# Kernel tuning notes

Measured on AMD Instinct MI355X. Metric: run time of the kernel, lower is better.

## Reference

```python
import jax, jax.numpy as jnp
import numpy as np

N_VIEWS = 3
N = 20000            # samples per omic view
NT = N_VIEWS * N     # homogeneous node count
E = 800000           # number of edges
R = 6                # num_relations
B = 4                # num_bases
H = 1                # heads
D = 128              # proj_dim == hidden_channels
IN_FEAT = 2000
NUM_LABELS = 5
NEG_SLOPE = 0.2      # PyG leaky_relu default slope


def setup_inputs() -> dict:
    key = jax.random.key(0)
    ks = jax.random.split(key, 16)
    inp = {}
    for i in range(N_VIEWS):
        inp[f"x{i}"] = jax.random.normal(ks[i], (N, IN_FEAT), jnp.float32)
        inp[f"w_proj{i}"] = jax.random.normal(ks[3 + i], (IN_FEAT, D), jnp.float32) / np.sqrt(IN_FEAT)
        inp[f"b_proj{i}"] = jnp.zeros((D,), jnp.float32)
    inp["edge_src"] = jax.random.randint(ks[6], (E,), 0, NT, jnp.int32)
    inp["edge_dst"] = jax.random.randint(ks[7], (E,), 0, NT, jnp.int32)
    inp["edge_type"] = jax.random.randint(ks[8], (E,), 0, R, jnp.int32)
    inp["basis"] = jax.random.normal(ks[9], (B, D, H * D), jnp.float32) / np.sqrt(D)
    inp["comp"] = jax.random.normal(ks[10], (R, B), jnp.float32) / np.sqrt(B)
    inp["att_q"] = jax.random.normal(ks[11], (H * D, H), jnp.float32) / np.sqrt(D)
    inp["att_k"] = jax.random.normal(ks[12], (H * D, H), jnp.float32) / np.sqrt(D)
    inp["conv_bias"] = jnp.zeros((H * D,), jnp.float32)
    inp["w_int"] = jax.random.normal(ks[13], (N_VIEWS * H * D, NUM_LABELS), jnp.float32) / np.sqrt(N_VIEWS * D)
    inp["b_int"] = jnp.zeros((NUM_LABELS,), jnp.float32)
    return inp


def rgat_conv(x, edge_src, edge_dst, edge_type, basis, comp, att_q, att_k, bias):
    """PyG RGATConv: basis-decomposed relational transform + additive
    across-relation self-attention (dim=1), sum aggregation, concat heads."""
    e = edge_src.shape[0]
    # relation weights from bases: [R, D, H*D]
    w = jnp.einsum('rb,bio->rio', comp, basis)
    # transform every node under every relation: [R, NT, H*D]
    xw = jnp.einsum('nd,rdo->rno', x, w)
    xi = xw[edge_type, edge_dst]   # [E, H*D] transformed target feats
    xj = xw[edge_type, edge_src]   # [E, H*D] transformed source feats
    q = xi @ att_q                 # [E, H]
    k = xj @ att_k                 # [E, H]
    alpha = jax.nn.leaky_relu(q + k, NEG_SLOPE)
    # softmax over incoming edges of each target node (across relations)
    amax = jax.lax.stop_gradient(jax.ops.segment_max(alpha, edge_dst, num_segments=NT))
    ealpha = jnp.exp(alpha - amax[edge_dst])
    denom = jax.ops.segment_sum(ealpha, edge_dst, num_segments=NT)
    alpha = ealpha / (denom[edge_dst] + 1e-16)
    msg = (xj.reshape(e, H, D) * alpha[:, :, None]).reshape(e, H * D)
    out = jax.ops.segment_sum(msg, edge_dst, num_segments=NT)  # [NT, H*D]
    return out + bias


def reference(x0, x1, x2, w_proj0, b_proj0, w_proj1, b_proj1, w_proj2, b_proj2,
              edge_src, edge_dst, edge_type, basis, comp, att_q, att_k,
              conv_bias, w_int, b_int):
    # per-omic projection + relu, then concat to homogeneous node matrix
    h = jnp.concatenate([
        jax.nn.relu(x0 @ w_proj0 + b_proj0),
        jax.nn.relu(x1 @ w_proj1 + b_proj1),
        jax.nn.relu(x2 @ w_proj2 + b_proj2),
    ], axis=0)                                        # [NT, D]
    h = jax.nn.relu(rgat_conv(h, edge_src, edge_dst, edge_type,
                              basis, comp, att_q, att_k, conv_bias))
    # node-type gather: nodes are ordered by type in the homogeneous graph
    views = h.reshape(N_VIEWS, N, H * D)              # [V, N, D]
    feat = jnp.transpose(views, (1, 0, 2)).reshape(N, N_VIEWS * H * D)
    # LinearIntegration: concat views -> linear to classes
    return feat @ w_int + b_int                        # [N, NUM_LABELS]
```

## Files before the change

### kernel.cpp

```cpp
#include <hip/hip_runtime.h>

#define NV 3
#define NN 20000
#define NTT 60000
#define NE 800000
#define NR 6
#define NB 4
#define DD 128
#define INF 2000
#define NL 5
#define LDT 40

typedef __attribute__((ext_vector_type(8))) short short8;
typedef __attribute__((ext_vector_type(4))) float f32x4;

__device__ __forceinline__ unsigned short f2bf(float f) {
    unsigned int u = __float_as_uint(f);
    u += 0x7FFFu + ((u >> 16) & 1u);
    return (unsigned short)(u >> 16);
}
__device__ __forceinline__ float bf2f(unsigned short h) {
    return __uint_as_float(((unsigned int)h) << 16);
}


__global__ void prep_wT(const float* __restrict__ w0, const float* __restrict__ w1,
                        const float* __restrict__ w2, unsigned short* __restrict__ wT) {
    int idx = blockIdx.x * 256 + threadIdx.x;
    if (idx >= NV * DD * INF) return;
    int v = idx / (DD * INF);
    int rem = idx - v * DD * INF;
    int n = rem / INF;
    int k = rem - n * INF;
    const float* w = (v == 0) ? w0 : ((v == 1) ? w1 : w2);
    wT[idx] = f2bf(w[(size_t)k * DD + n]);
}

__global__ void prep_wrel(const float* __restrict__ basis, const float* __restrict__ comp,
                          unsigned short* __restrict__ wTrel) {
    int idx = blockIdx.x * 256 + threadIdx.x;
    if (idx >= NR * DD * DD) return;
    int r = idx / (DD * DD);
    int rem = idx - r * DD * DD;
    int o = rem / DD;
    int d = rem - o * DD;
    float s = 0.f;
    #pragma unroll
    for (int b = 0; b < NB; b++) s += comp[r * NB + b] * basis[((size_t)b * DD + d) * DD + o];
    wTrel[idx] = f2bf(s);
}

__global__ void prep_qkvec(const float* __restrict__ basis, const float* __restrict__ comp,
                           const float* __restrict__ att_q, const float* __restrict__ att_k,
                           float* __restrict__ qvec, float* __restrict__ kvec) {
    int idx = blockIdx.x * 256 + threadIdx.x;
    if (idx >= 2 * NR * DD) return;
    int sel = idx / (NR * DD);
    int rem = idx - sel * (NR * DD);
    int r = rem / DD;
    int d = rem - r * DD;
    const float* att = sel ? att_k : att_q;
    float s = 0.f;
    #pragma unroll
    for (int b = 0; b < NB; b++) {
        float cb = comp[r * NB + b];
        float t = 0.f;
        for (int o = 0; o < DD; o++) t += basis[((size_t)b * DD + d) * DD + o] * att[o];
        s += cb * t;
    }
    (sel ? kvec : qvec)[r * DD + d] = s;
}

__global__ void zero2(int* __restrict__ a, int* __restrict__ b) {
    int i = blockIdx.x * 256 + threadIdx.x;
    if (i < NTT) { a[i] = 0; b[i] = 0; }
}

__global__ __launch_bounds__(256) void proj_gemm(
    const float* __restrict__ x0, const float* __restrict__ x1, const float* __restrict__ x2,
    const float* __restrict__ b0, const float* __restrict__ b1, const float* __restrict__ b2,
    const unsigned short* __restrict__ wT, unsigned short* __restrict__ hout) {
    __shared__ unsigned short lds_a[64 * LDT];
    __shared__ unsigned short lds_b[128 * LDT];
    int v = blockIdx.y;
    const float* x = (v == 0) ? x0 : ((v == 1) ? x1 : x2);
    const float* bias = (v == 0) ? b0 : ((v == 1) ? b1 : b2);
    const unsigned short* wTv = wT + (size_t)v * DD * INF;

    int t = threadIdx.x;
    int arow = t >> 2, aq = t & 3;
    int gr = blockIdx.x * 64 + arow;
    bool arowok = gr < NN;
    int brow = t >> 1, bh = t & 1;

    int lane = t & 63, wid = t >> 6;
    int wm = wid >> 1, wn = wid & 1;
    int lm = lane & 15, lq = lane >> 4;

    f32x4 acc[2][4];
    #pragma unroll
    for (int i = 0; i < 2; i++)
        #pragma unroll
        for (int j = 0; j < 4; j++) {
            acc[i][j][0] = 0.f; acc[i][j][1] = 0.f; acc[i][j][2] = 0.f; acc[i][j][3] = 0.f;
        }

    const int KT = (INF + 31) / 32;
    float4 fa0, fa1;
    uint4 fb0, fb1;

    auto loadA = [&](int kk) {
        int kb = kk * 32 + aq * 8;
        fa0 = make_float4(0.f, 0.f, 0.f, 0.f);
        fa1 = fa0;
        if (arowok && kb < INF) {
            const float4* p = (const float4*)(x + (size_t)gr * INF + kb);
            fa0 = p[0]; fa1 = p[1];
        }
    };
    auto loadB = [&](int kk) {
        int kb = kk * 32 + bh * 16;
        fb0 = make_uint4(0, 0, 0, 0);
        fb1 = fb0;
        if (kb < INF) {
            const uint4* p = (const uint4*)(wTv + (size_t)brow * INF + kb);
            fb0 = p[0]; fb1 = p[1];
        }
    };
    auto stage = [&]() {
        ushort4 u0, u1;
        u0.x = f2bf(fa0.x); u0.y = f2bf(fa0.y); u0.z = f2bf(fa0.z); u0.w = f2bf(fa0.w);
        u1.x = f2bf(fa1.x); u1.y = f2bf(fa1.y); u1.z = f2bf(fa1.z); u1.w = f2bf(fa1.w);
        *(ushort4*)&lds_a[arow * LDT + aq * 8] = u0;
        *(ushort4*)&lds_a[arow * LDT + aq * 8 + 4] = u1;
        *(uint4*)&lds_b[brow * LDT + bh * 16] = fb0;
        *(uint4*)&lds_b[brow * LDT + bh * 16 + 8] = fb1;
    };

    loadA(0); loadB(0);
    for (int kk = 0; kk < KT; kk++) {
        stage();
        __syncthreads();
        if (kk + 1 < KT) { loadA(kk + 1); loadB(kk + 1); }
        short8 af[2], bfr[4];
        #pragma unroll
        for (int i = 0; i < 2; i++)
            af[i] = *(const short8*)&lds_a[(wm * 32 + i * 16 + lm) * LDT + lq * 8];
        #pragma unroll
        for (int j = 0; j < 4; j++)
            bfr[j] = *(const short8*)&lds_b[(wn * 64 + j * 16 + lm) * LDT + lq * 8];
        #pragma unroll
        for (int i = 0; i < 2; i++)
            #pragma unroll
            for (int j = 0; j < 4; j++)
                acc[i][j] = __builtin_amdgcn_mfma_f32_16x16x32_bf16(af[i], bfr[j], acc[i][j], 0, 0, 0);
        __syncthreads();
    }
    #pragma unroll
    for (int i = 0; i < 2; i++) {
        int lr = wm * 32 + i * 16 + lq * 4;
        #pragma unroll
        for (int j = 0; j < 4; j++) {
            int c = wn * 64 + j * 16 + lm;
            float bv = bias[c];
            #pragma unroll
            for (int u = 0; u < 4; u++) {
                int grow = blockIdx.x * 64 + lr + u;
                if (grow < NN) {
                    float o = fmaxf(acc[i][j][u] + bv, 0.f);
                    hout[((size_t)(v * NN + grow)) * DD + c] = f2bf(o);
                }
            }
        }
    }
}

__global__ __launch_bounds__(256) void xw_gemm(
    const unsigned short* __restrict__ h, const unsigned short* __restrict__ wTrel,
    unsigned short* __restrict__ xw) {
    __shared__ unsigned short lds_a[128 * LDT];
    __shared__ unsigned short lds_b[128 * LDT];
    int r = blockIdx.y;
    const unsigned short* wTr = wTrel + (size_t)r * DD * DD;
    int t = threadIdx.x;
    int sr = t >> 1, sh = t & 1;
    int grow = blockIdx.x * 128 + sr;
    int grc = (grow < NTT) ? grow : (NTT - 1);
    int lane = t & 63, wid = t >> 6;
    int wm = wid >> 1, wn = wid & 1;
    int lm = lane & 15, lq = lane >> 4;

    f32x4 acc[4][4];
    #pragma unroll
    for (int i = 0; i < 4; i++)
        #pragma unroll
        for (int j = 0; j < 4; j++) {
            acc[i][j][0] = 0.f; acc[i][j][1] = 0.f; acc[i][j][2] = 0.f; acc[i][j][3] = 0.f;
        }

    #pragma unroll
    for (int kk = 0; kk < 4; kk++) {
        int k0 = kk * 32 + sh * 16;
        const uint4* asrc = (const uint4*)(h + (size_t)grc * DD + k0);
        *(uint4*)&lds_a[sr * LDT + sh * 16] = asrc[0];
        *(uint4*)&lds_a[sr * LDT + sh * 16 + 8] = asrc[1];
        const uint4* bsrc = (const uint4*)(wTr + (size_t)sr * DD + k0);
        *(uint4*)&lds_b[sr * LDT + sh * 16] = bsrc[0];
        *(uint4*)&lds_b[sr * LDT + sh * 16 + 8] = bsrc[1];
        __syncthreads();
        short8 af[4], bfr[4];
        #pragma unroll
        for (int i = 0; i < 4; i++)
            af[i] = *(const short8*)&lds_a[(wm * 64 + i * 16 + lm) * LDT + lq * 8];
        #pragma unroll
        for (int j = 0; j < 4; j++)
            bfr[j] = *(const short8*)&lds_b[(wn * 64 + j * 16 + lm) * LDT + lq * 8];
        #pragma unroll
        for (int i = 0; i < 4; i++)
            #pragma unroll
            for (int j = 0; j < 4; j++)
                acc[i][j] = __builtin_amdgcn_mfma_f32_16x16x32_bf16(af[i], bfr[j], acc[i][j], 0, 0, 0);
        __syncthreads();
    }
    #pragma unroll
    for (int i = 0; i < 4; i++) {
        int lr = wm * 64 + i * 16 + lq * 4;
        #pragma unroll
        for (int j = 0; j < 4; j++) {
            int c = wn * 64 + j * 16 + lm;
            #pragma unroll
            for (int u = 0; u < 4; u++) {
                int g2 = blockIdx.x * 128 + lr + u;
                if (g2 < NTT)
                    xw[((size_t)r * NTT + g2) * DD + c] = f2bf(acc[i][j][u]);
            }
        }
    }
}

__global__ void qk_nodes(const unsigned short* __restrict__ h, const float* __restrict__ qvec,
                         const float* __restrict__ kvec, float* __restrict__ qn,
                         float* __restrict__ kn) {
    int wid = threadIdx.x >> 6, lane = threadIdx.x & 63;
    int node = blockIdx.x * 4 + wid;
    if (node >= NTT) return;
    unsigned int u = *(const unsigned int*)(h + (size_t)node * DD + lane * 2);
    float h0 = bf2f(u & 0xffff), h1 = bf2f(u >> 16);
    #pragma unroll
    for (int r = 0; r < NR; r++) {
        float pq = h0 * qvec[r * DD + lane * 2] + h1 * qvec[r * DD + lane * 2 + 1];
        float pk = h0 * kvec[r * DD + lane * 2] + h1 * kvec[r * DD + lane * 2 + 1];
        #pragma unroll
        for (int off = 32; off; off >>= 1) {
            pq += __shfl_xor(pq, off);
            pk += __shfl_xor(pk, off);
        }
        if (lane == 0) {
            qn[r * NTT + node] = pq;
            kn[r * NTT + node] = pk;
        }
    }
}

__global__ void hist(const int* __restrict__ dst, int* __restrict__ indeg) {
    int e = blockIdx.x * 256 + threadIdx.x;
    if (e < NE) atomicAdd(&indeg[dst[e]], 1);
}

__global__ __launch_bounds__(1024) void scan_indeg(const int* __restrict__ indeg,
                                                   int* __restrict__ start) {
    int t = threadIdx.x;
    const int per = (NTT + 1023) / 1024;
    int base = t * per;
    int s = 0;
    for (int i = 0; i < per; i++) {
        int idx = base + i;
        if (idx < NTT) s += indeg[idx];
    }
    int lane = t & 63, wid = t >> 6;
    __shared__ int wsum[16];
    int v = s;
    #pragma unroll
    for (int off = 1; off < 64; off <<= 1) {
        int u = __shfl_up(v, off);
        if (lane >= off) v += u;
    }
    if (lane == 63) wsum[wid] = v;
    __syncthreads();
    if (t < 16) {
        int w = wsum[t];
        #pragma unroll
        for (int off = 1; off < 16; off <<= 1) {
            int u = __shfl_up(w, off);
            if (t >= off) w += u;
        }
        wsum[t] = w;
    }
    __syncthreads();
    int excl = (v - s) + (wid ? wsum[wid - 1] : 0);
    int run = excl;
    for (int i = 0; i < per; i++) {
        int idx = base + i;
        if (idx < NTT) {
            start[idx] = run;
            run += indeg[idx];
        }
    }
    if (t == 1023) start[NTT] = run;
}

__global__ void scatter2(const int* __restrict__ dst, const int* __restrict__ src,
                         const int* __restrict__ typ, const int* __restrict__ start,
                         int* __restrict__ cursor, const float* __restrict__ qn,
                         const float* __restrict__ kn, unsigned int* __restrict__ packed,
                         float* __restrict__ wl) {
    int e = blockIdx.x * 256 + threadIdx.x;
    if (e >= NE) return;
    int d = dst[e], ss = src[e], tt = typ[e];
    float al = qn[tt * NTT + d] + kn[tt * NTT + ss];
    al = (al > 0.f) ? al : 0.2f * al;
    float w = __expf(al);
    int pos = atomicAdd(&cursor[d], 1);
    int idx = start[d] + pos;
    packed[idx] = (unsigned)ss | ((unsigned)tt << 16);
    wl[idx] = w;
}

__global__ void aggregate(const unsigned int* __restrict__ packed, const float* __restrict__ wl,
                          const int* __restrict__ start, const unsigned short* __restrict__ xw,
                          const float* __restrict__ conv_bias, float* __restrict__ h2) {
    int wid = threadIdx.x >> 6, lane = threadIdx.x & 63;
    int node = blockIdx.x * 4 + wid;
    if (node >= NTT) return;
    int s0 = start[node], s1 = start[node + 1];
    float a0 = 0.f, a1 = 0.f, denom = 0.f;
    for (int base = s0; base < s1; base += 64) {
        int cnt = min(64, s1 - base);
        unsigned pk = 0;
        float wv = 0.f;
        if (lane < cnt) {
            pk = packed[base + lane];
            wv = wl[base + lane];
        }
        denom += wv;
        for (int i = 0; i < cnt; i++) {
            unsigned sp = __shfl(pk, i);
            float sw = __shfl(wv, i);
            unsigned ss = sp & 0xFFFFu;
            unsigned tt = sp >> 16;
            unsigned u = *(const unsigned int*)(xw + ((size_t)tt * NTT + ss) * DD + lane * 2);
            a0 += sw * bf2f(u & 0xffff);
            a1 += sw * bf2f(u >> 16);
        }
    }
    #pragma unroll
    for (int off = 32; off; off >>= 1) denom += __shfl_xor(denom, off);
    float rdenom = 1.f / (denom + 1e-16f);
    float2 o;
    o.x = fmaxf(a0 * rdenom + conv_bias[lane * 2], 0.f);
    o.y = fmaxf(a1 * rdenom + conv_bias[lane * 2 + 1], 0.f);
    *(float2*)&h2[(size_t)node * DD + lane * 2] = o;
}

__global__ void final_linear(const float* __restrict__ h2, const float* __restrict__ w_int,
                             const float* __restrict__ b_int, float* __restrict__ out) {
    int wid = threadIdx.x >> 6, lane = threadIdx.x & 63;
    int node = blockIdx.x * 4 + wid;
    if (node >= NN) return;
    float acc[NL] = {0.f, 0.f, 0.f, 0.f, 0.f};
    for (int j = lane; j < NV * DD; j += 64) {
        int v = j >> 7, d = j & 127;
        float f = h2[((size_t)(v * NN + node)) * DD + d];
        #pragma unroll
        for (int c = 0; c < NL; c++) acc[c] += f * w_int[j * NL + c];
    }
    #pragma unroll
    for (int c = 0; c < NL; c++) {
        float s = acc[c];
        #pragma unroll
        for (int off = 32; off; off >>= 1) s += __shfl_xor(s, off);
        if (lane == 0) out[(size_t)node * NL + c] = s + b_int[c];
    }
}

extern "C" void kernel_launch(void* const* d_in, const int* in_sizes, int n_in, void* d_out,
                              int out_size, void* d_ws, size_t ws_size, hipStream_t stream) {
    (void)in_sizes; (void)n_in; (void)out_size; (void)ws_size;
    const float* x0 = (const float*)d_in[0];
    const float* w0 = (const float*)d_in[1];
    const float* b0 = (const float*)d_in[2];
    const float* x1 = (const float*)d_in[3];
    const float* w1 = (const float*)d_in[4];
    const float* b1 = (const float*)d_in[5];
    const float* x2 = (const float*)d_in[6];
    const float* w2 = (const float*)d_in[7];
    const float* b2 = (const float*)d_in[8];
    const int* esrc = (const int*)d_in[9];
    const int* edst = (const int*)d_in[10];
    const int* etype = (const int*)d_in[11];
    const float* basis = (const float*)d_in[12];
    const float* comp = (const float*)d_in[13];
    const float* att_q = (const float*)d_in[14];
    const float* att_k = (const float*)d_in[15];
    const float* conv_bias = (const float*)d_in[16];
    const float* w_int = (const float*)d_in[17];
    const float* b_int = (const float*)d_in[18];

    char* ws = (char*)d_ws;
    size_t off = 0;
    auto alloc = [&](size_t bytes) -> void* {
        void* p = ws + off;
        off += bytes;
        off = (off + 255) & ~(size_t)255;
        return p;
    };
    unsigned short* h = (unsigned short*)alloc((size_t)NTT * DD * 2);
    unsigned short* xw = (unsigned short*)alloc((size_t)NR * NTT * DD * 2);
    float* qn = (float*)alloc((size_t)NR * NTT * 4);
    float* kn = (float*)alloc((size_t)NR * NTT * 4);
    unsigned short* wT = (unsigned short*)alloc((size_t)NV * DD * INF * 2);
    unsigned short* wTrel = (unsigned short*)alloc((size_t)NR * DD * DD * 2);
    float* qvec = (float*)alloc((size_t)NR * DD * 4);
    float* kvec = (float*)alloc((size_t)NR * DD * 4);
    int* indeg = (int*)alloc((size_t)NTT * 4);
    int* cursor = (int*)alloc((size_t)NTT * 4);
    int* startp = (int*)alloc((size_t)(NTT + 1) * 4);
    unsigned int* packed = (unsigned int*)alloc((size_t)NE * 4);
    float* wl = (float*)alloc((size_t)NE * 4);
    float* h2 = (float*)alloc((size_t)NTT * DD * 4);

    prep_wT<<<(NV * DD * INF + 255) / 256, 256, 0, stream>>>(w0, w1, w2, wT);
    prep_wrel<<<(NR * DD * DD + 255) / 256, 256, 0, stream>>>(basis, comp, wTrel);
    prep_qkvec<<<(2 * NR * DD + 255) / 256, 256, 0, stream>>>(basis, comp, att_q, att_k, qvec, kvec);
    zero2<<<(NTT + 255) / 256, 256, 0, stream>>>(indeg, cursor);

    proj_gemm<<<dim3((NN + 63) / 64, NV), 256, 0, stream>>>(x0, x1, x2, b0, b1, b2, wT, h);
    qk_nodes<<<(NTT + 3) / 4, 256, 0, stream>>>(h, qvec, kvec, qn, kn);
    xw_gemm<<<dim3((NTT + 127) / 128, NR), 256, 0, stream>>>(h, wTrel, xw);

    hist<<<(NE + 255) / 256, 256, 0, stream>>>(edst, indeg);
    scan_indeg<<<1, 1024, 0, stream>>>(indeg, startp);
    scatter2<<<(NE + 255) / 256, 256, 0, stream>>>(edst, esrc, etype, startp, cursor, qn, kn,
                                                   packed, wl);

    aggregate<<<(NTT + 3) / 4, 256, 0, stream>>>(packed, wl, startp, xw, conv_bias, h2);
    final_linear<<<(NN + 3) / 4, 256, 0, stream>>>(h2, w_int, b_int, (float*)d_out);
}
```

Before: 899.5 us.

## Drop LDS staging in GEMMs, tile weight transpose, merge prep kernels

The projection and relation GEMMs no longer stage through LDS. Each lane now loads its MFMA fragments straight from global memory, and the projection tile grows from 64 to 128 rows. The weight transpose goes through a shared-memory tile so both reads and writes are coalesced. The small prep kernels and the zeroing kernel are merged into one launch, and the graph histogram and scan are moved ahead of the GEMMs. This removes barriers and LDS traffic and cuts launches, but each wave now fetches its own fragments from L2, which can raise global memory traffic on the large x reads.

After: 948.2 us. +5.4%, slower.

```diff
diff --git a/kernel.cpp b/kernel.cpp
--- a/kernel.cpp
+++ b/kernel.cpp
@@ -1,4 +1,5 @@
 #include <hip/hip_runtime.h>
+#include <hip/hip_bf16.h>
 
 #define NV 3
 #define NN 20000
@@ -9,7 +10,6 @@
 #define DD 128
 #define INF 2000
 #define NL 5
-#define LDT 40
 
 typedef __attribute__((ext_vector_type(8))) short short8;
 typedef __attribute__((ext_vector_type(4))) float f32x4;
@@ -22,150 +22,157 @@
 __device__ __forceinline__ float bf2f(unsigned short h) {
     return __uint_as_float(((unsigned int)h) << 16);
 }
-
-
-__global__ void prep_wT(const float* __restrict__ w0, const float* __restrict__ w1,
-                        const float* __restrict__ w2, unsigned short* __restrict__ wT) {
-    int idx = blockIdx.x * 256 + threadIdx.x;
-    if (idx >= NV * DD * INF) return;
-    int v = idx / (DD * INF);
-    int rem = idx - v * DD * INF;
-    int n = rem / INF;
-    int k = rem - n * INF;
+__device__ __forceinline__ short8 cvt8(float4 a, float4 b) {
+    union { short8 v; __hip_bfloat162 h[4]; } u;
+    u.h[0] = __float22bfloat162_rn(make_float2(a.x, a.y));
+    u.h[1] = __float22bfloat162_rn(make_float2(a.z, a.w));
+    u.h[2] = __float22bfloat162_rn(make_float2(b.x, b.y));
+    u.h[3] = __float22bfloat162_rn(make_float2(b.z, b.w));
+    return u.v;
+}
+
+__global__ void prep_misc(const float* __restrict__ basis, const float* __restrict__ comp,
+                          const float* __restrict__ att_q, const float* __restrict__ att_k,
+                          unsigned short* __restrict__ wTrel, float* __restrict__ qvec,
+                          float* __restrict__ kvec, int* __restrict__ indeg,
+                          int* __restrict__ cursor) {
+    int b = blockIdx.x;
+    if (b < 384) {
+        int idx = b * 256 + threadIdx.x;
+        int r = idx / (DD * DD);
+        int rem = idx - r * (DD * DD);
+        int o = rem / DD;
+        int d = rem - o * DD;
+        float s = 0.f;
+        #pragma unroll
+        for (int bb = 0; bb < NB; bb++)
+            s += comp[r * NB + bb] * basis[((size_t)bb * DD + d) * DD + o];
+        wTrel[idx] = f2bf(s);
+    } else if (b < 390) {
+        int idx = (b - 384) * 256 + threadIdx.x;
+        int sel = idx / (NR * DD);
+        int rem = idx - sel * (NR * DD);
+        int r = rem / DD;
+        int d = rem - r * DD;
+        const float* att = sel ? att_k : att_q;
+        float s = 0.f;
+        #pragma unroll
+        for (int bb = 0; bb < NB; bb++) {
+            float cb = comp[r * NB + bb];
+            float t = 0.f;
+            for (int o = 0; o < DD; o++) t += basis[((size_t)bb * DD + d) * DD + o] * att[o];
+            s += cb * t;
+        }
+        (sel ? kvec : qvec)[r * DD + d] = s;
+    } else {
+        int i = (b - 390) * 256 + threadIdx.x;
+        if (i < NTT) { indeg[i] = 0; cursor[i] = 0; }
+    }
+}
+
+__global__ void prep_wTt(const float* __restrict__ w0, const float* __restrict__ w1,
+                         const float* __restrict__ w2, unsigned short* __restrict__ wT) {
+    __shared__ float tile[32][33];
+    int v = blockIdx.z;
     const float* w = (v == 0) ? w0 : ((v == 1) ? w1 : w2);
-    wT[idx] = f2bf(w[(size_t)k * DD + n]);
-}
-
-__global__ void prep_wrel(const float* __restrict__ basis, const float* __restrict__ comp,
-                          unsigned short* __restrict__ wTrel) {
-    int idx = blockIdx.x * 256 + threadIdx.x;
-    if (idx >= NR * DD * DD) return;
-    int r = idx / (DD * DD);
-    int rem = idx - r * DD * DD;
-    int o = rem / DD;
-    int d = rem - o * DD;
-    float s = 0.f;
-    #pragma unroll
-    for (int b = 0; b < NB; b++) s += comp[r * NB + b] * basis[((size_t)b * DD + d) * DD + o];
-    wTrel[idx] = f2bf(s);
-}
-
-__global__ void prep_qkvec(const float* __restrict__ basis, const float* __restrict__ comp,
-                           const float* __restrict__ att_q, const float* __restrict__ att_k,
-                           float* __restrict__ qvec, float* __restrict__ kvec) {
-    int idx = blockIdx.x * 256 + threadIdx.x;
-    if (idx >= 2 * NR * DD) return;
-    int sel = idx / (NR * DD);
-    int rem = idx - sel * (NR * DD);
-    int r = rem / DD;
-    int d = rem - r * DD;
-    const float* att = sel ? att_k : att_q;
-    float s = 0.f;
-    #pragma unroll
-    for (int b = 0; b < NB; b++) {
-        float cb = comp[r * NB + b];
-        float t = 0.f;
-        for (int o = 0; o < DD; o++) t += basis[((size_t)b * DD + d) * DD + o] * att[o];
-        s += cb * t;
-    }
-    (sel ? kvec : qvec)[r * DD + d] = s;
-}
-
-__global__ void zero2(int* __restrict__ a, int* __restrict__ b) {
-    int i = blockIdx.x * 256 + threadIdx.x;
-    if (i < NTT) { a[i] = 0; b[i] = 0; }
-}
-
-__global__ __launch_bounds__(256) void proj_gemm(
+    int k0 = blockIdx.x * 32, n0 = blockIdx.y * 32;
+    int tx = threadIdx.x & 31, ty = threadIdx.x >> 5;
+    #pragma unroll
+    for (int i = 0; i < 4; i++) {
+        int k = k0 + ty + i * 8;
+        if (k < INF) tile[ty + i * 8][tx] = w[(size_t)k * DD + n0 + tx];
+    }
+    __syncthreads();
+    #pragma unroll
+    for (int i = 0; i < 4; i++) {
+        int k = k0 + tx;
+        int n = n0 + ty + i * 8;
+        if (k < INF)
+            wT[(size_t)v * DD * INF + (size_t)n * INF + k] = f2bf(tile[tx][ty + i * 8]);
+    }
+}
+
+__global__ __launch_bounds__(256) void proj_nl(
     const float* __restrict__ x0, const float* __restrict__ x1, const float* __restrict__ x2,
     const float* __restrict__ b0, const float* __restrict__ b1, const float* __restrict__ b2,
     const unsigned short* __restrict__ wT, unsigned short* __restrict__ hout) {
-    __shared__ unsigned short lds_a[64 * LDT];
-    __shared__ unsigned short lds_b[128 * LDT];
     int v = blockIdx.y;
     const float* x = (v == 0) ? x0 : ((v == 1) ? x1 : x2);
     const float* bias = (v == 0) ? b0 : ((v == 1) ? b1 : b2);
     const unsigned short* wTv = wT + (size_t)v * DD * INF;
 
-    int t = threadIdx.x;
-    int arow = t >> 2, aq = t & 3;
-    int gr = blockIdx.x * 64 + arow;
-    bool arowok = gr < NN;
-    int brow = t >> 1, bh = t & 1;
-
-    int lane = t & 63, wid = t >> 6;
+    int t = threadIdx.x, lane = t & 63, wid = t >> 6;
     int wm = wid >> 1, wn = wid & 1;
     int lm = lane & 15, lq = lane >> 4;
 
-    f32x4 acc[2][4];
-    #pragma unroll
-    for (int i = 0; i < 2; i++)
+    const float* aptr[4];
+    #pragma unroll
+    for (int i = 0; i < 4; i++) {
+        int r = blockIdx.x * 128 + wm * 64 + i * 16 + lm;
+        if (r >= NN) r = NN - 1;
+        aptr[i] = x + (size_t)r * INF + lq * 8;
+    }
+    const unsigned short* bptr[4];
+    #pragma unroll
+    for (int j = 0; j < 4; j++) {
+        int c = wn * 64 + j * 16 + lm;
+        bptr[j] = wTv + (size_t)c * INF + lq * 8;
+    }
+
+    f32x4 acc[4][4];
+    #pragma unroll
+    for (int i = 0; i < 4; i++)
         #pragma unroll
         for (int j = 0; j < 4; j++) {
             acc[i][j][0] = 0.f; acc[i][j][1] = 0.f; acc[i][j][2] = 0.f; acc[i][j][3] = 0.f;
         }
 
-    const int KT = (INF + 31) / 32;
-    float4 fa0, fa1;
-    uint4 fb0, fb1;
-
-    auto loadA = [&](int kk) {
-        int kb = kk * 32 + aq * 8;
-        fa0 = make_float4(0.f, 0.f, 0.f, 0.f);
-        fa1 = fa0;
-        if (arowok && kb < INF) {
-            const float4* p = (const float4*)(x + (size_t)gr * INF + kb);
-            fa0 = p[0]; fa1 = p[1];
-        }
-    };
-    auto loadB = [&](int kk) {
-        int kb = kk * 32 + bh * 16;
-        fb0 = make_uint4(0, 0, 0, 0);
-        fb1 = fb0;
-        if (kb < INF) {
-            const uint4* p = (const uint4*)(wTv + (size_t)brow * INF + kb);
-            fb0 = p[0]; fb1 = p[1];
-        }
-    };
-    auto stage = [&]() {
-        ushort4 u0, u1;
-        u0.x = f2bf(fa0.x); u0.y = f2bf(fa0.y); u0.z = f2bf(fa0.z); u0.w = f2bf(fa0.w);
-        u1.x = f2bf(fa1.x); u1.y = f2bf(fa1.y); u1.z = f2bf(fa1.z); u1.w = f2bf(fa1.w);
-        *(ushort4*)&lds_a[arow * LDT + aq * 8] = u0;
-        *(ushort4*)&lds_a[arow * LDT + aq * 8 + 4] = u1;
-        *(uint4*)&lds_b[brow * LDT + bh * 16] = fb0;
-        *(uint4*)&lds_b[brow * LDT + bh * 16 + 8] = fb1;
-    };
-
-    loadA(0); loadB(0);
-    for (int kk = 0; kk < KT; kk++) {
-        stage();
-        __syncthreads();
-        if (kk + 1 < KT) { loadA(kk + 1); loadB(kk + 1); }
-        short8 af[2], bfr[4];
-        #pragma unroll
-        for (int i = 0; i < 2; i++)
-            af[i] = *(const short8*)&lds_a[(wm * 32 + i * 16 + lm) * LDT + lq * 8];
+    #pragma unroll 2
+    for (int kk = 0; kk < 62; kk++) {
+        short8 af[4], bfr[4];
+        #pragma unroll
+        for (int i = 0; i < 4; i++) {
+            const float4* p = (const float4*)(aptr[i] + kk * 32);
+            af[i] = cvt8(p[0], p[1]);
+        }
         #pragma unroll
         for (int j = 0; j < 4; j++)
-            bfr[j] = *(const short8*)&lds_b[(wn * 64 + j * 16 + lm) * LDT + lq * 8];
-        #pragma unroll
-        for (int i = 0; i < 2; i++)
+            bfr[j] = *(const short8*)(bptr[j] + kk * 32);
+        #pragma unroll
+        for (int i = 0; i < 4; i++)
             #pragma unroll
             for (int j = 0; j < 4; j++)
                 acc[i][j] = __builtin_amdgcn_mfma_f32_16x16x32_bf16(af[i], bfr[j], acc[i][j], 0, 0, 0);
-        __syncthreads();
-    }
-    #pragma unroll
-    for (int i = 0; i < 2; i++) {
-        int lr = wm * 32 + i * 16 + lq * 4;
+    }
+    {
+        short8 af[4], bfr[4];
+        short8 z = {0, 0, 0, 0, 0, 0, 0, 0};
+        #pragma unroll
+        for (int i = 0; i < 4; i++) {
+            if (lq < 2) {
+                const float4* p = (const float4*)(aptr[i] + 62 * 32);
+                af[i] = cvt8(p[0], p[1]);
+            } else af[i] = z;
+        }
+        #pragma unroll
+        for (int j = 0; j < 4; j++)
+            bfr[j] = (lq < 2) ? *(const short8*)(bptr[j] + 62 * 32) : z;
+        #pragma unroll
+        for (int i = 0; i < 4; i++)
+            #pragma unroll
+            for (int j = 0; j < 4; j++)
+                acc[i][j] = __builtin_amdgcn_mfma_f32_16x16x32_bf16(af[i], bfr[j], acc[i][j], 0, 0, 0);
+    }
+    #pragma unroll
+    for (int i = 0; i < 4; i++) {
+        int lr = wm * 64 + i * 16 + lq * 4;
         #pragma unroll
         for (int j = 0; j < 4; j++) {
             int c = wn * 64 + j * 16 + lm;
             float bv = bias[c];
             #pragma unroll
             for (int u = 0; u < 4; u++) {
-                int grow = blockIdx.x * 64 + lr + u;
+                int grow = blockIdx.x * 128 + lr + u;
                 if (grow < NN) {
                     float o = fmaxf(acc[i][j][u] + bv, 0.f);
                     hout[((size_t)(v * NN + grow)) * DD + c] = f2bf(o);
@@ -175,21 +182,29 @@
     }
 }
 
-__global__ __launch_bounds__(256) void xw_gemm(
+__global__ __launch_bounds__(256) void xw_nl(
     const unsigned short* __restrict__ h, const unsigned short* __restrict__ wTrel,
     unsigned short* __restrict__ xw) {
-    __shared__ unsigned short lds_a[128 * LDT];
-    __shared__ unsigned short lds_b[128 * LDT];
     int r = blockIdx.y;
     const unsigned short* wTr = wTrel + (size_t)r * DD * DD;
-    int t = threadIdx.x;
-    int sr = t >> 1, sh = t & 1;
-    int grow = blockIdx.x * 128 + sr;
-    int grc = (grow < NTT) ? grow : (NTT - 1);
-    int lane = t & 63, wid = t >> 6;
+    int t = threadIdx.x, lane = t & 63, wid = t >> 6;
     int wm = wid >> 1, wn = wid & 1;
     int lm = lane & 15, lq = lane >> 4;
 
+    const unsigned short* aptr[4];
+    #pragma unroll
+    for (int i = 0; i < 4; i++) {
+        int rr = blockIdx.x * 128 + wm * 64 + i * 16 + lm;
+        if (rr >= NTT) rr = NTT - 1;
+        aptr[i] = h + (size_t)rr * DD + lq * 8;
+    }
+    const unsigned short* bptr[4];
+    #pragma unroll
+    for (int j = 0; j < 4; j++) {
+        int c = wn * 64 + j * 16 + lm;
+        bptr[j] = wTr + (size_t)c * DD + lq * 8;
+    }
+
     f32x4 acc[4][4];
     #pragma unroll
     for (int i = 0; i < 4; i++)
@@ -200,27 +215,16 @@
 
     #pragma unroll
     for (int kk = 0; kk < 4; kk++) {
-        int k0 = kk * 32 + sh * 16;
-        const uint4* asrc = (const uint4*)(h + (size_t)grc * DD + k0);
-        *(uint4*)&lds_a[sr * LDT + sh * 16] = asrc[0];
-        *(uint4*)&lds_a[sr * LDT + sh * 16 + 8] = asrc[1];
-        const uint4* bsrc = (const uint4*)(wTr + (size_t)sr * DD + k0);
-        *(uint4*)&lds_b[sr * LDT + sh * 16] = bsrc[0];
-        *(uint4*)&lds_b[sr * LDT + sh * 16 + 8] = bsrc[1];
-        __syncthreads();
         short8 af[4], bfr[4];
         #pragma unroll
-        for (int i = 0; i < 4; i++)
-            af[i] = *(const short8*)&lds_a[(wm * 64 + i * 16 + lm) * LDT + lq * 8];
-        #pragma unroll
-        for (int j = 0; j < 4; j++)
-            bfr[j] = *(const short8*)&lds_b[(wn * 64 + j * 16 + lm) * LDT + lq * 8];
+        for (int i = 0; i < 4; i++) af[i] = *(const short8*)(aptr[i] + kk * 32);
+        #pragma unroll
+        for (int j = 0; j < 4; j++) bfr[j] = *(const short8*)(bptr[j] + kk * 32);
         #pragma unroll
         for (int i = 0; i < 4; i++)
             #pragma unroll
             for (int j = 0; j < 4; j++)
                 acc[i][j] = __builtin_amdgcn_mfma_f32_16x16x32_bf16(af[i], bfr[j], acc[i][j], 0, 0, 0);
-        __syncthreads();
     }
     #pragma unroll
     for (int i = 0; i < 4; i++) {
@@ -429,20 +433,18 @@
     float* wl = (float*)alloc((size_t)NE * 4);
     float* h2 = (float*)alloc((size_t)NTT * DD * 4);
 
-    prep_wT<<<(NV * DD * INF + 255) / 256, 256, 0, stream>>>(w0, w1, w2, wT);
-    prep_wrel<<<(NR * DD * DD + 255) / 256, 256, 0, stream>>>(basis, comp, wTrel);
-    prep_qkvec<<<(2 * NR * DD + 255) / 256, 256, 0, stream>>>(basis, comp, att_q, att_k, qvec, kvec);
-    zero2<<<(NTT + 255) / 256, 256, 0, stream>>>(indeg, cursor);
-
-    proj_gemm<<<dim3((NN + 63) / 64, NV), 256, 0, stream>>>(x0, x1, x2, b0, b1, b2, wT, h);
-    qk_nodes<<<(NTT + 3) / 4, 256, 0, stream>>>(h, qvec, kvec, qn, kn);
-    xw_gemm<<<dim3((NTT + 127) / 128, NR), 256, 0, stream>>>(h, wTrel, xw);
-
+    prep_misc<<<390 + (NTT + 255) / 256, 256, 0, stream>>>(basis, comp, att_q, att_k, wTrel,
+                                                           qvec, kvec, indeg, cursor);
+    prep_wTt<<<dim3((INF + 31) / 32, DD / 32, NV), 256, 0, stream>>>(w0, w1, w2, wT);
     hist<<<(NE + 255) / 256, 256, 0, stream>>>(edst, indeg);
     scan_indeg<<<1, 1024, 0, stream>>>(indeg, startp);
+
+    proj_nl<<<dim3((NN + 127) / 128, NV), 256, 0, stream>>>(x0, x1, x2, b0, b1, b2, wT, h);
+    qk_nodes<<<(NTT + 3) / 4, 256, 0, stream>>>(h, qvec, kvec, qn, kn);
+    xw_nl<<<dim3((NTT + 127) / 128, NR), 256, 0, stream>>>(h, wTrel, xw);
+
     scatter2<<<(NE + 255) / 256, 256, 0, stream>>>(edst, esrc, etype, startp, cursor, qn, kn,
                                                    packed, wl);
-
     aggregate<<<(NTT + 3) / 4, 256, 0, stream>>>(packed, wl, startp, xw, conv_bias, h2);
     final_linear<<<(NN + 3) / 4, 256, 0, stream>>>(h2, w_int, b_int, (float*)d_out);
 }
```
